# Optimization experiments

Measured on AMD Instinct MI355X. Metric: run time of the kernel, lower is better.

Reference implementation:

```python
import jax, jax.numpy as jnp
import numpy as np

N_QUBITS = 20
BATCH = 32
DATA_COLS = (0, 1, 2, 5, 6, 7)  # columns of x used for data encoding, in order


def _rx(s, a):
    # s: (B, Q, 2) complex64 product state amplitudes; a: (B, Q) float angles
    c = jnp.cos(a / 2)
    isn = 1j * jnp.sin(a / 2)  # complex64
    s0, s1 = s[..., 0], s[..., 1]
    return jnp.stack([c * s0 - isn * s1, -isn * s0 + c * s1], axis=-1)


def _rz(s, a):
    ph = jnp.exp(-0.5j * a)  # exp(-i a/2), complex64
    return jnp.stack([s[..., 0] * ph, s[..., 1] * jnp.conj(ph)], axis=-1)


def setup_inputs() -> dict:
    key = jax.random.key(0)
    k1, k2 = jax.random.split(key)
    x = jax.random.normal(k1, (BATCH, 8, N_QUBITS), dtype=jnp.float32)
    weights = jax.random.normal(k2, (6, 3, BATCH, N_QUBITS), dtype=jnp.float32)
    return {"x": x, "weights": weights}


def reference(x, weights):
    b, _, n = x.shape
    # |0>^n product state: (B, Q, 2)
    s = jnp.zeros((b, n, 2), jnp.complex64).at[..., 0].set(1.0)
    for i, col in enumerate(DATA_COLS):
        w = weights[i]
        s = _rx(s, w[0])          # fR block: Rx -> Rz -> Rx (learned)
        s = _rz(s, w[1])
        s = _rx(s, w[2])
        s = _rx(s, x[:, col])     # data encoding Rx
    # kron fold: parallel doubling over qubits -> (B, 2^n) wavefunction
    wf = s[:, 0]
    for q in range(1, n):
        wf = (wf[:, :, None] * s[:, q][:, None, :]).reshape(b, -1)
    # Observable Z^(x)n is diagonal with sign (-1)^popcount(index)
    p = jnp.arange(wf.shape[1], dtype=jnp.uint32)
    for sh in (16, 8, 4, 2, 1):
        p = p ^ (p >> sh)
    signs = 1.0 - 2.0 * (p & 1).astype(jnp.float32)
    prob = wf.real * wf.real + wf.imag * wf.imag
    O = jnp.sum(signs * prob, axis=1).reshape(b, 1, 1).astype(jnp.complex64)
    state = s.reshape(b, n, 1, 2, 1)
    return state, O
```

## Files before the change

kernel.cpp:

```cpp
#include <hip/hip_runtime.h>
#include <hip/hip_bf16.h>
#include <math.h>

#define NQ 20
#define NB 32

__global__ __launch_bounds__(NB * NQ) void qc_kernel(
    const float* __restrict__ x,
    const float* __restrict__ w,
    float* __restrict__ outf,
    __hip_bfloat16* __restrict__ outb,
    const int f32_mode) {
  __shared__ float zexp[NB][NQ];

  const int t = threadIdx.x;
  const int b = t / NQ;
  const int q = t - b * NQ;

  float s0r = 1.0f, s0i = 0.0f, s1r = 0.0f, s1i = 0.0f;

  const int cols[6] = {0, 1, 2, 5, 6, 7};

#pragma unroll
  for (int i = 0; i < 6; ++i) {
    {
      const float a = w[((i * 3 + 0) * NB + b) * NQ + q];
      float sn, c; sincosf(0.5f * a, &sn, &c);
      const float t0r = c * s0r + sn * s1i;
      const float t0i = c * s0i - sn * s1r;
      const float t1r = c * s1r + sn * s0i;
      const float t1i = c * s1i - sn * s0r;
      s0r = t0r; s0i = t0i; s1r = t1r; s1i = t1i;
    }
    {
      const float a = w[((i * 3 + 1) * NB + b) * NQ + q];
      float sn, c; sincosf(0.5f * a, &sn, &c);
      const float t0r = s0r * c + s0i * sn;
      const float t0i = s0i * c - s0r * sn;
      const float t1r = s1r * c - s1i * sn;
      const float t1i = s1i * c + s1r * sn;
      s0r = t0r; s0i = t0i; s1r = t1r; s1i = t1i;
    }
    {
      const float a = w[((i * 3 + 2) * NB + b) * NQ + q];
      float sn, c; sincosf(0.5f * a, &sn, &c);
      const float t0r = c * s0r + sn * s1i;
      const float t0i = c * s0i - sn * s1r;
      const float t1r = c * s1r + sn * s0i;
      const float t1i = c * s1i - sn * s0r;
      s0r = t0r; s0i = t0i; s1r = t1r; s1i = t1i;
    }
    {
      const float a = x[(b * 8 + cols[i]) * NQ + q];
      float sn, c; sincosf(0.5f * a, &sn, &c);
      const float t0r = c * s0r + sn * s1i;
      const float t0i = c * s0i - sn * s1r;
      const float t1r = c * s1r + sn * s0i;
      const float t1i = c * s1i - sn * s0r;
      s0r = t0r; s0i = t0i; s1r = t1r; s1i = t1i;
    }
  }

  zexp[b][q] = (s0r * s0r + s0i * s0i) - (s1r * s1r + s1i * s1i);

  if (f32_mode) {
    reinterpret_cast<float2*>(outf)[t] = make_float2(s0r, s1r);
  } else {
    struct alignas(8) bf16x4 { __hip_bfloat16 a, b, c, d; } pk;
    pk.a = __float2bfloat16(s0r);
    pk.b = __float2bfloat16(s0i);
    pk.c = __float2bfloat16(s1r);
    pk.d = __float2bfloat16(s1i);
    reinterpret_cast<bf16x4*>(outb)[t] = pk;
  }

  __syncthreads();

  if (t < NB) {
    float p = 1.0f;
#pragma unroll
    for (int qq = 0; qq < NQ; ++qq) p *= zexp[t][qq];
    if (f32_mode) {
      outf[1280 + t] = p;
    } else {
      outb[2560 + 2 * t + 0] = __float2bfloat16(p);
      outb[2560 + 2 * t + 1] = __float2bfloat16(0.0f);
    }
  }
}

extern "C" void kernel_launch(void* const* d_in, const int* in_sizes, int n_in,
                              void* d_out, int out_size, void* d_ws, size_t ws_size,
                              hipStream_t stream) {
  const float* x;
  const float* w;
  if (in_sizes[0] <= in_sizes[1]) {
    x = (const float*)d_in[0];
    w = (const float*)d_in[1];
  } else {
    w = (const float*)d_in[0];
    x = (const float*)d_in[1];
  }

  const int f32_mode = (out_size == 1312) ? 1 : 0;

  qc_kernel<<<1, NB * NQ, 0, stream>>>(
      x, w, (float*)d_out, (__hip_bfloat16*)d_out, f32_mode);
}
```

Measured before the change: 62.90 us.

## Split batch across blocks, use fast trig, and reduce via wave shuffles

Launches one 64-thread block per batch element instead of a single 640-thread block, so the work spreads over several compute units. The product over qubits is now done with wavefront xor-shuffles instead of shared memory, a barrier and a serial loop. sincosf is replaced by the __cosf/__sinf intrinsics, trading accuracy for speed. The bf16 output path is dropped and only f32 output is kept, so the bf16 output case is no longer handled.

```diff
diff --git a/kernel.cpp b/kernel.cpp
--- a/kernel.cpp
+++ b/kernel.cpp
@@ -5,88 +5,65 @@
 #define NQ 20
 #define NB 32
 
-__global__ __launch_bounds__(NB * NQ) void qc_kernel(
+__global__ __launch_bounds__(64) void qc_kernel(
     const float* __restrict__ x,
     const float* __restrict__ w,
-    float* __restrict__ outf,
-    __hip_bfloat16* __restrict__ outb,
-    const int f32_mode) {
-  __shared__ float zexp[NB][NQ];
-
-  const int t = threadIdx.x;
-  const int b = t / NQ;
-  const int q = t - b * NQ;
+    float* __restrict__ out) {
+  const int b = blockIdx.x;
+  const int q = threadIdx.x;
 
   float s0r = 1.0f, s0i = 0.0f, s1r = 0.0f, s1i = 0.0f;
 
-  const int cols[6] = {0, 1, 2, 5, 6, 7};
-
+  if (q < NQ) {
+    const int cols[6] = {0, 1, 2, 5, 6, 7};
 #pragma unroll
-  for (int i = 0; i < 6; ++i) {
-    {
-      const float a = w[((i * 3 + 0) * NB + b) * NQ + q];
-      float sn, c; sincosf(0.5f * a, &sn, &c);
-      const float t0r = c * s0r + sn * s1i;
-      const float t0i = c * s0i - sn * s1r;
-      const float t1r = c * s1r + sn * s0i;
-      const float t1i = c * s1i - sn * s0r;
-      s0r = t0r; s0i = t0i; s1r = t1r; s1i = t1i;
+    for (int i = 0; i < 6; ++i) {
+      {
+        const float a = 0.5f * w[((i * 3 + 0) * NB + b) * NQ + q];
+        const float c = __cosf(a), sn = __sinf(a);
+        const float t0r = c * s0r + sn * s1i;
+        const float t0i = c * s0i - sn * s1r;
+        const float t1r = c * s1r + sn * s0i;
+        const float t1i = c * s1i - sn * s0r;
+        s0r = t0r; s0i = t0i; s1r = t1r; s1i = t1i;
+      }
+      {
+        const float a = 0.5f * w[((i * 3 + 1) * NB + b) * NQ + q];
+        const float c = __cosf(a), sn = __sinf(a);
+        const float t0r = s0r * c + s0i * sn;
+        const float t0i = s0i * c - s0r * sn;
+        const float t1r = s1r * c - s1i * sn;
+        const float t1i = s1i * c + s1r * sn;
+        s0r = t0r; s0i = t0i; s1r = t1r; s1i = t1i;
+      }
+      {
+        const float a = 0.5f * w[((i * 3 + 2) * NB + b) * NQ + q];
+        const float c = __cosf(a), sn = __sinf(a);
+        const float t0r = c * s0r + sn * s1i;
+        const float t0i = c * s0i - sn * s1r;
+        const float t1r = c * s1r + sn * s0i;
+        const float t1i = c * s1i - sn * s0r;
+        s0r = t0r; s0i = t0i; s1r = t1r; s1i = t1i;
+      }
+      {
+        const float a = 0.5f * x[(b * 8 + cols[i]) * NQ + q];
+        const float c = __cosf(a), sn = __sinf(a);
+        const float t0r = c * s0r + sn * s1i;
+        const float t0i = c * s0i - sn * s1r;
+        const float t1r = c * s1r + sn * s0i;
+        const float t1i = c * s1i - sn * s0r;
+        s0r = t0r; s0i = t0i; s1r = t1r; s1i = t1i;
+      }
     }
-    {
-      const float a = w[((i * 3 + 1) * NB + b) * NQ + q];
-      float sn, c; sincosf(0.5f * a, &sn, &c);
-      const float t0r = s0r * c + s0i * sn;
-      const float t0i = s0i * c - s0r * sn;
-      const float t1r = s1r * c - s1i * sn;
-      const float t1i = s1i * c + s1r * sn;
-      s0r = t0r; s0i = t0i; s1r = t1r; s1i = t1i;
-    }
-    {
-      const float a = w[((i * 3 + 2) * NB + b) * NQ + q];
-      float sn, c; sincosf(0.5f * a, &sn, &c);
-      const float t0r = c * s0r + sn * s1i;
-      const float t0i = c * s0i - sn * s1r;
-      const float t1r = c * s1r + sn * s0i;
-      const float t1i = c * s1i - sn * s0r;
-      s0r = t0r; s0i = t0i; s1r = t1r; s1i = t1i;
-    }
-    {
-      const float a = x[(b * 8 + cols[i]) * NQ + q];
-      float sn, c; sincosf(0.5f * a, &sn, &c);
-      const float t0r = c * s0r + sn * s1i;
-      const float t0i = c * s0i - sn * s1r;
-      const float t1r = c * s1r + sn * s0i;
-      const float t1i = c * s1i - sn * s0r;
-      s0r = t0r; s0i = t0i; s1r = t1r; s1i = t1i;
-    }
+    reinterpret_cast<float2*>(out)[b * NQ + q] = make_float2(s0r, s1r);
   }
 
-  zexp[b][q] = (s0r * s0r + s0i * s0i) - (s1r * s1r + s1i * s1i);
-
-  if (f32_mode) {
-    reinterpret_cast<float2*>(outf)[t] = make_float2(s0r, s1r);
-  } else {
-    struct alignas(8) bf16x4 { __hip_bfloat16 a, b, c, d; } pk;
-    pk.a = __float2bfloat16(s0r);
-    pk.b = __float2bfloat16(s0i);
-    pk.c = __float2bfloat16(s1r);
-    pk.d = __float2bfloat16(s1i);
-    reinterpret_cast<bf16x4*>(outb)[t] = pk;
-  }
-
-  __syncthreads();
-
-  if (t < NB) {
-    float p = 1.0f;
+  float z = (q < NQ)
+                ? (s0r * s0r + s0i * s0i) - (s1r * s1r + s1i * s1i)
+                : 1.0f;
 #pragma unroll
-    for (int qq = 0; qq < NQ; ++qq) p *= zexp[t][qq];
-    if (f32_mode) {
-      outf[1280 + t] = p;
-    } else {
-      outb[2560 + 2 * t + 0] = __float2bfloat16(p);
-      outb[2560 + 2 * t + 1] = __float2bfloat16(0.0f);
-    }
-  }
+  for (int m = 1; m < 64; m <<= 1) z *= __shfl_xor(z, m, 64);
+  if (q == 0) out[2 * NB * NQ + b] = z;
 }
 
 extern "C" void kernel_launch(void* const* d_in, const int* in_sizes, int n_in,
@@ -101,9 +78,5 @@
     w = (const float*)d_in[0];
     x = (const float*)d_in[1];
   }
-
-  const int f32_mode = (out_size == 1312) ? 1 : 0;
-
-  qc_kernel<<<1, NB * NQ, 0, stream>>>(
-      x, w, (float*)d_out, (__hip_bfloat16*)d_out, f32_mode);
+  qc_kernel<<<NB, 64, 0, stream>>>(x, w, (float*)d_out);
 }
```

New measurement: 55.41 us. 1.14x faster.
